# Kernel optimization log

Hardware: AMD Instinct MI355X
Metric: run time of the kernel (lower is better)

## Reference

```python
import jax, jax.numpy as jnp
import numpy as np

B, N, DIM = 16, 1024, 512
H, DH = 8, 64  # heads, dim_head; inner_dim = H*DH = 512
MASK_VAL = -1e-9  # value ASSIGNED (not added) to diagonal, per original code


def setup_inputs() -> dict:
    key = jax.random.key(0)
    ks = jax.random.split(key, 8)
    w = 0.02  # small init so softmax is not saturated
    x = jax.random.normal(ks[0], (B, N, DIM), dtype=jnp.float32)
    Wq = jax.random.normal(ks[1], (DIM, H * DH), dtype=jnp.float32) * w
    Wkv = jax.random.normal(ks[2], (DIM, 2 * H * DH), dtype=jnp.float32) * w
    scale = jnp.full((H,), DH ** -0.5, dtype=jnp.float32)  # nn.Parameter(scale*ones(heads))
    mix_pre = jax.random.normal(ks[3], (H, H), dtype=jnp.float32) * w
    mix_post = jax.random.normal(ks[4], (H, H), dtype=jnp.float32) * w
    Wout = jax.random.normal(ks[5], (H * DH, DIM), dtype=jnp.float32) * w
    bout = jnp.zeros((DIM,), dtype=jnp.float32)
    return {"x": x, "Wq": Wq, "Wkv": Wkv, "scale": scale,
            "mix_pre": mix_pre, "mix_post": mix_post, "Wout": Wout, "bout": bout}


def reference(x, Wq, Wkv, scale, mix_pre, mix_post, Wout, bout):
    b, n, _ = x.shape
    # projections -> [b, h, n, d]
    q = (x @ Wq).reshape(b, n, H, DH).transpose(0, 2, 1, 3)
    kv = (x @ Wkv).reshape(b, n, 2, H, DH)
    k = kv[:, :, 0].transpose(0, 2, 1, 3)
    v = kv[:, :, 1].transpose(0, 2, 1, 3)
    # LMSA: per-head learned scale
    dots = jnp.einsum('bhid,bhjd->bhij', q, k) * scale[None, :, None, None]
    # if_patch_attn: set diagonal entries to -1e-9 (assignment, as in torch)
    eye = jnp.eye(n, dtype=bool)
    dots = jnp.where(eye, jnp.float32(MASK_VAL), dots)
    # talking heads: pre-softmax head mix
    dots = jnp.einsum('bhij,hg->bgij', dots, mix_pre)
    attn = jax.nn.softmax(dots, axis=-1)
    # post-softmax head mix
    attn = jnp.einsum('bhij,hg->bgij', attn, mix_post)
    out = jnp.einsum('bhij,bhjd->bhid', attn, v)  # [b,h,n,d]
    out = out.transpose(0, 2, 1, 3).reshape(b, n, H * DH)
    return out @ Wout + bout
```

## Files before the change

kernel.cpp:

```cpp
#include <hip/hip_runtime.h>
#include <math.h>


typedef short bf16x8 __attribute__((ext_vector_type(8)));
typedef float f32x4 __attribute__((ext_vector_type(4)));

__device__ __forceinline__ f32x4 mfma16(bf16x8 a, bf16x8 b, f32x4 c) {
  return __builtin_amdgcn_mfma_f32_16x16x32_bf16(a, b, c, 0, 0, 0);
}

__device__ __forceinline__ unsigned short f2bf(float f) {
  unsigned u = __float_as_uint(f);
  u = (u + 0x7fffu + ((u >> 16) & 1u)) >> 16;
  return (unsigned short)u;
}

__device__ __forceinline__ void splitbf(float f, unsigned short& hi,
                                        unsigned short& lo) {
  hi = f2bf(f);
  float fh = __uint_as_float((unsigned)hi << 16);
  lo = f2bf(f - fh);
}

__device__ __forceinline__ f32x4 zero4() {
  f32x4 z = {0.f, 0.f, 0.f, 0.f};
  return z;
}

namespace {

constexpr int kB = 16, kN = 1024, kH = 8;

__global__ __launch_bounds__(256) void zero_f32(float* __restrict__ p) {
  int id = blockIdx.x * 256 + threadIdx.x;
  ((float4*)p)[id] = make_float4(0.f, 0.f, 0.f, 0.f);
}

__global__ __launch_bounds__(256) void prep(
    const float* __restrict__ Wq, const float* __restrict__ Wkv,
    const float* __restrict__ Wout, unsigned short* __restrict__ WTh,
    unsigned short* __restrict__ WTl, unsigned short* __restrict__ WoTh,
    unsigned short* __restrict__ WoTl) {
  int id = blockIdx.x * 256 + threadIdx.x;
  unsigned short h, l;
  if (id < 1536 * 512) {
    int n = id >> 9, k = id & 511;
    float v = (n < 512) ? Wq[(size_t)k * 512 + n]
                        : Wkv[(size_t)k * 1024 + (n - 512)];
    splitbf(v, h, l);
    WTh[id] = h; WTl[id] = l;
  } else {
    int id2 = id - 1536 * 512;
    int n = id2 >> 9, k = id2 & 511;
    splitbf(Wout[(size_t)k * 512 + n], h, l);
    WoTh[id2] = h; WoTl[id2] = l;
  }
}

__global__ __launch_bounds__(256) void gemm_qkv(
    const float* __restrict__ X, const unsigned short* __restrict__ WTh,
    const unsigned short* __restrict__ WTl, const float* __restrict__ scale,
    unsigned short* __restrict__ Qh, unsigned short* __restrict__ Ql,
    unsigned short* __restrict__ Kh, unsigned short* __restrict__ Kl,
    unsigned short* __restrict__ Vh, unsigned short* __restrict__ Vl) {
  __shared__ unsigned short Ah[128 * 72], Al[128 * 72];
  __shared__ unsigned short Bh[128 * 72], Bl[128 * 72];
  const int tid = threadIdx.x;
  const int n0 = blockIdx.x * 128, m0 = blockIdx.y * 128;
  const int w = tid >> 6, lane = tid & 63, quad = lane >> 4, ln = lane & 15;
  const int mw = (w >> 1) * 64, nw = (w & 1) * 64;
  const int srow = tid >> 3, schk = (tid & 7) * 8;
  f32x4 acc[4][4];
#pragma unroll
  for (int i = 0; i < 4; ++i)
#pragma unroll
    for (int j = 0; j < 4; ++j) acc[i][j] = zero4();
  for (int k0 = 0; k0 < 512; k0 += 64) {
    float xa[4][8];
    uint4 bh4[4], bl4[4];
#pragma unroll
    for (int c2 = 0; c2 < 4; ++c2) {
      const float* xs = X + (size_t)(m0 + c2 * 32 + srow) * 512 + k0 + schk;
      *(float4*)&xa[c2][0] = *(const float4*)xs;
      *(float4*)&xa[c2][4] = *(const float4*)(xs + 4);
      size_t boff = (size_t)(n0 + c2 * 32 + srow) * 512 + k0 + schk;
      bh4[c2] = *(const uint4*)(WTh + boff);
      bl4[c2] = *(const uint4*)(WTl + boff);
    }
    __syncthreads();
#pragma unroll
    for (int c2 = 0; c2 < 4; ++c2) {
      unsigned short hh[8], ll[8];
#pragma unroll
      for (int e = 0; e < 8; ++e) splitbf(xa[c2][e], hh[e], ll[e]);
      uint4 ph, pl;
      ph.x = hh[0] | ((unsigned)hh[1] << 16); pl.x = ll[0] | ((unsigned)ll[1] << 16);
      ph.y = hh[2] | ((unsigned)hh[3] << 16); pl.y = ll[2] | ((unsigned)ll[3] << 16);
      ph.z = hh[4] | ((unsigned)hh[5] << 16); pl.z = ll[4] | ((unsigned)ll[5] << 16);
      ph.w = hh[6] | ((unsigned)hh[7] << 16); pl.w = ll[6] | ((unsigned)ll[7] << 16);
      *(uint4*)&Ah[(c2 * 32 + srow) * 72 + schk] = ph;
      *(uint4*)&Al[(c2 * 32 + srow) * 72 + schk] = pl;
      *(uint4*)&Bh[(c2 * 32 + srow) * 72 + schk] = bh4[c2];
      *(uint4*)&Bl[(c2 * 32 + srow) * 72 + schk] = bl4[c2];
    }
    __syncthreads();
#pragma unroll
    for (int ks = 0; ks < 2; ++ks) {
      bf16x8 afh[4], afl[4], bfh[4], bfl[4];
#pragma unroll
      for (int t = 0; t < 4; ++t) {
        int ao = (mw + t * 16 + ln) * 72 + ks * 32 + quad * 8;
        int bo = (nw + t * 16 + ln) * 72 + ks * 32 + quad * 8;
        afh[t] = *(const bf16x8*)&Ah[ao];
        afl[t] = *(const bf16x8*)&Al[ao];
        bfh[t] = *(const bf16x8*)&Bh[bo];
        bfl[t] = *(const bf16x8*)&Bl[bo];
      }
#pragma unroll
      for (int mt = 0; mt < 4; ++mt)
#pragma unroll
        for (int nt = 0; nt < 4; ++nt) {
          acc[mt][nt] = mfma16(afh[mt], bfh[nt], acc[mt][nt]);
          acc[mt][nt] = mfma16(afh[mt], bfl[nt], acc[mt][nt]);
          acc[mt][nt] = mfma16(afl[mt], bfh[nt], acc[mt][nt]);
        }
    }
  }
  const int region = n0 >> 9;
#pragma unroll
  for (int nt = 0; nt < 4; ++nt) {
    const int col = n0 + nw + nt * 16 + ln;
    const int local = col - region * 512;
    const int hh = local >> 6, d = local & 63;
    const float sc = (region == 0) ? scale[hh] : 1.f;
#pragma unroll
    for (int mt = 0; mt < 4; ++mt) {
#pragma unroll
      for (int r = 0; r < 4; ++r) {
        const int row = m0 + mw + mt * 16 + quad * 4 + r;
        const int b = row >> 10, i = row & 1023;
        unsigned short vh, vl;
        splitbf(acc[mt][nt][r] * sc, vh, vl);
        if (region == 0) {
          size_t o = (((size_t)(b * 8 + hh) * 1024 + i) << 6) + d;
          Qh[o] = vh; Ql[o] = vl;
        } else if (region == 1) {
          size_t o = (((size_t)(b * 8 + hh) * 1024 + i) << 6) + d;
          Kh[o] = vh; Kl[o] = vl;
        } else {
          size_t o = (((size_t)(b * 8 + hh) * 64 + d) << 10) + i;
          Vh[o] = vh; Vl[o] = vl;
        }
      }
    }
  }
}

__global__ __launch_bounds__(256) void attn_stats(
    const unsigned short* __restrict__ Qh_g, const unsigned short* __restrict__ Ql_g,
    const unsigned short* __restrict__ Kh, const unsigned short* __restrict__ Kl,
    const float* __restrict__ mix_pre, float* __restrict__ Lst) {
  __shared__ unsigned short Qsh[256 * 72];
  __shared__ float mixp_s[64], dfix_s[8];
  const int tid = threadIdx.x;
  const int b = blockIdx.y;
  const int i0 = (blockIdx.x >> 1) * 32;
  const int jb = (blockIdx.x & 1) * 512;
  const int w = tid >> 6, lane = tid & 63, quad = lane >> 4, ln = lane & 15;
  const int ih = (w >> 1) * 16, jh = (w & 1) * 16;
  if (tid < 64) mixp_s[tid] = mix_pre[tid];
  if (tid < 8) {
    float s = 0.f;
#pragma unroll
    for (int h = 0; h < 8; ++h) s += mix_pre[h * 8 + tid];
    dfix_s[tid] = -1e-9f * s;
  }
#pragma unroll
  for (int c = 0; c < 8; ++c) {
    int v = tid + 256 * c;
    int row = v >> 3, chk = (v & 7) * 8;
    int h = row >> 5, ii = row & 31;
    *(uint4*)&Qsh[row * 72 + chk] =
        *(const uint4*)(Qh_g + (((size_t)(b * 8 + h) * 1024 + i0 + ii) << 6) + chk);
  }
  bf16x8 qlo[8][2];
#pragma unroll
  for (int h = 0; h < 8; ++h)
#pragma unroll
    for (int ks = 0; ks < 2; ++ks)
      qlo[h][ks] = *(const bf16x8*)(
          Ql_g + (((size_t)(b * 8 + h) * 1024 + i0 + ih + ln) << 6) + ks * 32 + quad * 8);
  __syncthreads();
  float l[8][4];
#pragma unroll
  for (int a = 0; a < 8; ++a)
#pragma unroll
    for (int r = 0; r < 4; ++r) l[a][r] = 0.f;
  const int ig0 = i0 + ih + quad * 4;
  for (int j0 = jb; j0 < jb + 512; j0 += 32) {
    bf16x8 kh_r[2][2], kl_r[2][2];
#pragma unroll
    for (int ks = 0; ks < 2; ++ks) {
      size_t kro = (((size_t)(b * 8 + 0) * 1024 + j0 + jh + ln) << 6) + ks * 32 + quad * 8;
      kh_r[0][ks] = *(const bf16x8*)(Kh + kro);
      kl_r[0][ks] = *(const bf16x8*)(Kl + kro);
    }
    f32x4 S[8];
    int cur = 0;
#pragma unroll
    for (int h = 0; h < 8; ++h) {
      const int nxt = cur ^ 1;
      if (h < 7) {
#pragma unroll
        for (int ks = 0; ks < 2; ++ks) {
          size_t kro = (((size_t)(b * 8 + h + 1) * 1024 + j0 + jh + ln) << 6) + ks * 32 + quad * 8;
          kh_r[nxt][ks] = *(const bf16x8*)(Kh + kro);
          kl_r[nxt][ks] = *(const bf16x8*)(Kl + kro);
        }
      }
      f32x4 acc = zero4();
#pragma unroll
      for (int ks = 0; ks < 2; ++ks) {
        bf16x8 ah = *(const bf16x8*)&Qsh[(h * 32 + ih + ln) * 72 + ks * 32 + quad * 8];
        acc = mfma16(ah, kh_r[cur][ks], acc);
        acc = mfma16(ah, kl_r[cur][ks], acc);
        acc = mfma16(qlo[h][ks], kh_r[cur][ks], acc);
      }
      S[h] = acc;
      cur = nxt;
    }
    const int dr = (j0 + jh + ln) - ig0;
#pragma unroll
    for (int a = 0; a < 8; ++a) {
      f32x4 sm = S[0] * mixp_s[a];
#pragma unroll
      for (int h = 1; h < 8; ++h) sm += S[h] * mixp_s[h * 8 + a];
      const float df = dfix_s[a];
#pragma unroll
      for (int r = 0; r < 4; ++r) {
        float v = (r == dr) ? df : sm[r];
        l[a][r] += __expf(v);
      }
    }
  }
#pragma unroll
  for (int off = 1; off < 16; off <<= 1)
#pragma unroll
    for (int a = 0; a < 8; ++a)
#pragma unroll
      for (int r = 0; r < 4; ++r) l[a][r] += __shfl_xor(l[a][r], off);
  if (ln == 0) {
#pragma unroll
    for (int a = 0; a < 8; ++a)
#pragma unroll
      for (int r = 0; r < 4; ++r)
        atomicAdd(&Lst[(size_t)(b * 8 + a) * 1024 + ig0 + r], l[a][r]);
  }
}

__global__ __launch_bounds__(256) void attn_out(
    const unsigned short* __restrict__ Qh_g, const unsigned short* __restrict__ Ql_g,
    const unsigned short* __restrict__ Kh, const unsigned short* __restrict__ Kl,
    const unsigned short* __restrict__ Vh, const unsigned short* __restrict__ Vl,
    const float* __restrict__ mix_pre, const float* __restrict__ mix_post,
    const float* __restrict__ Lst, float* __restrict__ OAp) {
  __shared__ unsigned short Qsh[256 * 72];
  __shared__ unsigned short Wsh[256 * 40], Wsl[256 * 40];
  __shared__ float mixp_s[64], mixq_s[64], dfix_s[8];
  __shared__ float Ils[8][32];
  const int tid = threadIdx.x;
  const int b = blockIdx.y;
  const int i0 = (blockIdx.x >> 1) * 32;
  const int jb = (blockIdx.x & 1) * 512;
  float* OA = OAp + (size_t)(blockIdx.x & 1) * ((size_t)kB * kN * 512);
  const int w = tid >> 6, lane = tid & 63, quad = lane >> 4, ln = lane & 15;
  const int ih = (w >> 1) * 16, jh = (w & 1) * 16;
  if (tid < 64) { mixp_s[tid] = mix_pre[tid]; mixq_s[tid] = mix_post[tid]; }
  if (tid < 8) {
    float s = 0.f;
#pragma unroll
    for (int h = 0; h < 8; ++h) s += mix_pre[h * 8 + tid];
    dfix_s[tid] = -1e-9f * s;
  }
  {
    const int a = tid >> 5, row = tid & 31;
    Ils[a][row] = 1.f / Lst[(size_t)(b * 8 + a) * 1024 + i0 + row];
  }
#pragma unroll
  for (int c = 0; c < 8; ++c) {
    int v = tid + 256 * c;
    int row = v >> 3, chk = (v & 7) * 8;
    int h = row >> 5, ii = row & 31;
    *(uint4*)&Qsh[row * 72 + chk] =
        *(const uint4*)(Qh_g + (((size_t)(b * 8 + h) * 1024 + i0 + ii) << 6) + chk);
  }
  bf16x8 qlo[8][2];
#pragma unroll
  for (int h = 0; h < 8; ++h)
#pragma unroll
    for (int ks = 0; ks < 2; ++ks)
      qlo[h][ks] = *(const bf16x8*)(
          Ql_g + (((size_t)(b * 8 + h) * 1024 + i0 + ih + ln) << 6) + ks * 32 + quad * 8);
  __syncthreads();
  f32x4 O[2][2][4];
#pragma unroll
  for (int cc = 0; cc < 2; ++cc)
#pragma unroll
    for (int mt = 0; mt < 2; ++mt)
#pragma unroll
      for (int nt = 0; nt < 4; ++nt) O[cc][mt][nt] = zero4();
  const int ig0l = ih + quad * 4;
  for (int j0 = jb; j0 < jb + 512; j0 += 32) {
    bf16x8 kh_r[2][2], kl_r[2][2];
#pragma unroll
    for (int ks = 0; ks < 2; ++ks) {
      size_t kro = (((size_t)(b * 8 + 0) * 1024 + j0 + jh + ln) << 6) + ks * 32 + quad * 8;
      kh_r[0][ks] = *(const bf16x8*)(Kh + kro);
      kl_r[0][ks] = *(const bf16x8*)(Kl + kro);
    }
    f32x4 S[8];
    int cur = 0;
#pragma unroll
    for (int h = 0; h < 8; ++h) {
      const int nxt = cur ^ 1;
      if (h < 7) {
#pragma unroll
        for (int ks = 0; ks < 2; ++ks) {
          size_t kro = (((size_t)(b * 8 + h + 1) * 1024 + j0 + jh + ln) << 6) + ks * 32 + quad * 8;
          kh_r[nxt][ks] = *(const bf16x8*)(Kh + kro);
          kl_r[nxt][ks] = *(const bf16x8*)(Kl + kro);
        }
      }
      f32x4 acc = zero4();
#pragma unroll
      for (int ks = 0; ks < 2; ++ks) {
        bf16x8 ah = *(const bf16x8*)&Qsh[(h * 32 + ih + ln) * 72 + ks * 32 + quad * 8];
        acc = mfma16(ah, kh_r[cur][ks], acc);
        acc = mfma16(ah, kl_r[cur][ks], acc);
        acc = mfma16(qlo[h][ks], kh_r[cur][ks], acc);
      }
      S[h] = acc;
      cur = nxt;
    }
    const int dr = (j0 + jh + ln) - (i0 + ig0l);
    f32x4 P[8];
#pragma unroll
    for (int a = 0; a < 8; ++a) {
      f32x4 sm = S[0] * mixp_s[a];
#pragma unroll
      for (int h = 1; h < 8; ++h) sm += S[h] * mixp_s[h * 8 + a];
      const float df = dfix_s[a];
      f32x4 p;
#pragma unroll
      for (int r = 0; r < 4; ++r) {
        float v = (r == dr) ? df : sm[r];
        p[r] = __expf(v) * Ils[a][ig0l + r];
      }
      P[a] = p;
    }
#pragma unroll
    for (int c = 0; c < 8; ++c) {
      f32x4 wv = P[0] * mixq_s[c];
#pragma unroll
      for (int a = 1; a < 8; ++a) wv += P[a] * mixq_s[a * 8 + c];
#pragma unroll
      for (int r = 0; r < 4; ++r) {
        unsigned short vh, vl;
        splitbf(wv[r], vh, vl);
        int o = (c * 32 + ig0l + r) * 40 + jh + ln;
        Wsh[o] = vh; Wsl[o] = vl;
      }
    }
    __syncthreads();
#pragma unroll
    for (int cc = 0; cc < 2; ++cc) {
      const int c = w * 2 + cc;
      bf16x8 a0h = *(const bf16x8*)&Wsh[(c * 32 + ln) * 40 + quad * 8];
      bf16x8 a0l = *(const bf16x8*)&Wsl[(c * 32 + ln) * 40 + quad * 8];
      bf16x8 a1h = *(const bf16x8*)&Wsh[(c * 32 + 16 + ln) * 40 + quad * 8];
      bf16x8 a1l = *(const bf16x8*)&Wsl[(c * 32 + 16 + ln) * 40 + quad * 8];
#pragma unroll
      for (int nt = 0; nt < 4; ++nt) {
        size_t vo = (((size_t)(b * 8 + c) * 64 + nt * 16 + ln) << 10) + j0 + quad * 8;
        bf16x8 bvh = *(const bf16x8*)(Vh + vo);
        bf16x8 bvl = *(const bf16x8*)(Vl + vo);
        O[cc][0][nt] = mfma16(a0h, bvh, O[cc][0][nt]);
        O[cc][0][nt] = mfma16(a0h, bvl, O[cc][0][nt]);
        O[cc][0][nt] = mfma16(a0l, bvh, O[cc][0][nt]);
        O[cc][1][nt] = mfma16(a1h, bvh, O[cc][1][nt]);
        O[cc][1][nt] = mfma16(a1h, bvl, O[cc][1][nt]);
        O[cc][1][nt] = mfma16(a1l, bvh, O[cc][1][nt]);
      }
    }
    __syncthreads();
  }
#pragma unroll
  for (int cc = 0; cc < 2; ++cc)
#pragma unroll
    for (int mt = 0; mt < 2; ++mt)
#pragma unroll
      for (int nt = 0; nt < 4; ++nt)
#pragma unroll
        for (int r = 0; r < 4; ++r) {
          const int i = i0 + mt * 16 + quad * 4 + r;
          const int col = (w * 2 + cc) * 64 + nt * 16 + ln;
          OA[((size_t)(b * 1024 + i) << 9) + col] = O[cc][mt][nt][r];
        }
}

__global__ __launch_bounds__(256) void gemm_out(
    const float* __restrict__ A0, const float* __restrict__ A1,
    const unsigned short* __restrict__ BTh, const unsigned short* __restrict__ BTl,
    const float* __restrict__ bias, float* __restrict__ Out) {
  __shared__ unsigned short Ah[128 * 72], Al[128 * 72];
  __shared__ unsigned short Bh[128 * 72], Bl[128 * 72];
  const int tid = threadIdx.x;
  const int n0 = blockIdx.x * 128, m0 = blockIdx.y * 128;
  const int w = tid >> 6, lane = tid & 63, quad = lane >> 4, ln = lane & 15;
  const int mw = (w >> 1) * 64, nw = (w & 1) * 64;
  const int srow = tid >> 3, schk = (tid & 7) * 8;
  f32x4 acc[4][4];
#pragma unroll
  for (int i = 0; i < 4; ++i)
#pragma unroll
    for (int j = 0; j < 4; ++j) acc[i][j] = zero4();
  for (int k0 = 0; k0 < 512; k0 += 64) {
    float xa[4][8];
    uint4 bh4[4], bl4[4];
#pragma unroll
    for (int c2 = 0; c2 < 4; ++c2) {
      size_t aoff = (size_t)(m0 + c2 * 32 + srow) * 512 + k0 + schk;
      float4 a00 = *(const float4*)(A0 + aoff);
      float4 a01 = *(const float4*)(A0 + aoff + 4);
      float4 a10 = *(const float4*)(A1 + aoff);
      float4 a11 = *(const float4*)(A1 + aoff + 4);
      xa[c2][0] = a00.x + a10.x; xa[c2][1] = a00.y + a10.y;
      xa[c2][2] = a00.z + a10.z; xa[c2][3] = a00.w + a10.w;
      xa[c2][4] = a01.x + a11.x; xa[c2][5] = a01.y + a11.y;
      xa[c2][6] = a01.z + a11.z; xa[c2][7] = a01.w + a11.w;
      size_t boff = (size_t)(n0 + c2 * 32 + srow) * 512 + k0 + schk;
      bh4[c2] = *(const uint4*)(BTh + boff);
      bl4[c2] = *(const uint4*)(BTl + boff);
    }
    __syncthreads();
#pragma unroll
    for (int c2 = 0; c2 < 4; ++c2) {
      unsigned short hh[8], ll[8];
#pragma unroll
      for (int e = 0; e < 8; ++e) splitbf(xa[c2][e], hh[e], ll[e]);
      uint4 ph, pl;
      ph.x = hh[0] | ((unsigned)hh[1] << 16); pl.x = ll[0] | ((unsigned)ll[1] << 16);
      ph.y = hh[2] | ((unsigned)hh[3] << 16); pl.y = ll[2] | ((unsigned)ll[3] << 16);
      ph.z = hh[4] | ((unsigned)hh[5] << 16); pl.z = ll[4] | ((unsigned)ll[5] << 16);
      ph.w = hh[6] | ((unsigned)hh[7] << 16); pl.w = ll[6] | ((unsigned)ll[7] << 16);
      *(uint4*)&Ah[(c2 * 32 + srow) * 72 + schk] = ph;
      *(uint4*)&Al[(c2 * 32 + srow) * 72 + schk] = pl;
      *(uint4*)&Bh[(c2 * 32 + srow) * 72 + schk] = bh4[c2];
      *(uint4*)&Bl[(c2 * 32 + srow) * 72 + schk] = bl4[c2];
    }
    __syncthreads();
#pragma unroll
    for (int ks = 0; ks < 2; ++ks) {
      bf16x8 afh[4], afl[4], bfh[4], bfl[4];
#pragma unroll
      for (int t = 0; t < 4; ++t) {
        int ao = (mw + t * 16 + ln) * 72 + ks * 32 + quad * 8;
        int bo = (nw + t * 16 + ln) * 72 + ks * 32 + quad * 8;
        afh[t] = *(const bf16x8*)&Ah[ao];
        afl[t] = *(const bf16x8*)&Al[ao];
        bfh[t] = *(const bf16x8*)&Bh[bo];
        bfl[t] = *(const bf16x8*)&Bl[bo];
      }
#pragma unroll
      for (int mt = 0; mt < 4; ++mt)
#pragma unroll
        for (int nt = 0; nt < 4; ++nt) {
          acc[mt][nt] = mfma16(afh[mt], bfh[nt], acc[mt][nt]);
          acc[mt][nt] = mfma16(afh[mt], bfl[nt], acc[mt][nt]);
          acc[mt][nt] = mfma16(afl[mt], bfh[nt], acc[mt][nt]);
        }
    }
  }
#pragma unroll
  for (int nt = 0; nt < 4; ++nt) {
    const int col = n0 + nw + nt * 16 + ln;
    const float bcol = bias[col];
#pragma unroll
    for (int mt = 0; mt < 4; ++mt) {
#pragma unroll
      for (int r = 0; r < 4; ++r) {
        const int row = m0 + mw + mt * 16 + quad * 4 + r;
        Out[(size_t)row * 512 + col] = acc[mt][nt][r] + bcol;
      }
    }
  }
}

}

extern "C" void kernel_launch(void* const* d_in, const int* in_sizes, int n_in,
                              void* d_out, int out_size, void* d_ws, size_t ws_size,
                              hipStream_t stream) {
  const float* x        = (const float*)d_in[0];
  const float* Wq       = (const float*)d_in[1];
  const float* Wkv      = (const float*)d_in[2];
  const float* scale    = (const float*)d_in[3];
  const float* mix_pre  = (const float*)d_in[4];
  const float* mix_post = (const float*)d_in[5];
  const float* Wout     = (const float*)d_in[6];
  const float* bout     = (const float*)d_in[7];
  float* out = (float*)d_out;

  char* p = (char*)d_ws;
  const size_t qsz = (size_t)kB * kH * kN * 64;
  unsigned short* WTh  = (unsigned short*)p; p += (size_t)1536 * 512 * 2;
  unsigned short* WTl  = (unsigned short*)p; p += (size_t)1536 * 512 * 2;
  unsigned short* WoTh = (unsigned short*)p; p += (size_t)512 * 512 * 2;
  unsigned short* WoTl = (unsigned short*)p; p += (size_t)512 * 512 * 2;
  unsigned short* Qh   = (unsigned short*)p; p += qsz * 2;
  unsigned short* Ql   = (unsigned short*)p; p += qsz * 2;
  unsigned short* Kh   = (unsigned short*)p; p += qsz * 2;
  unsigned short* Kl   = (unsigned short*)p; p += qsz * 2;
  unsigned short* Vh   = (unsigned short*)p; p += qsz * 2;
  unsigned short* Vl   = (unsigned short*)p; p += qsz * 2;
  float* OAp = (float*)p; p += (size_t)2 * kB * kN * 512 * 4;
  float* Lst = (float*)p; p += (size_t)kB * kH * kN * 4;

  prep<<<4096, 256, 0, stream>>>(Wq, Wkv, Wout, WTh, WTl, WoTh, WoTl);
  gemm_qkv<<<dim3(12, 128), 256, 0, stream>>>(x, WTh, WTl, scale,
                                              Qh, Ql, Kh, Kl, Vh, Vl);
  zero_f32<<<128, 256, 0, stream>>>(Lst);
  attn_stats<<<dim3(64, 16), 256, 0, stream>>>(Qh, Ql, Kh, Kl, mix_pre, Lst);
  attn_out<<<dim3(64, 16), 256, 0, stream>>>(Qh, Ql, Kh, Kl, Vh, Vl, mix_pre,
                                             mix_post, Lst, OAp);
  gemm_out<<<dim3(4, 128), 256, 0, stream>>>(OAp, OAp + (size_t)kB * kN * 512,
                                             WoTh, WoTl, bout, out);
}
```

Baseline: 1.582 ms.

## Fuse softmax-stats and output attention passes into one kernel per query tile

Merges attn_stats and attn_out into a single kernel. Each 128-thread block now covers 16 query rows and the full key range. Row sums are reduced in shared memory instead of via atomics into a global buffer, which removes the zero-fill kernel, the atomics and the split-j partial output buffers that gemm_out had to add together. The trade-off is fewer threads per block (two waves) with a serial 1024-key loop, so each block does more sequential work and parallelism per block drops. V loads are double-buffered across heads.

```diff
diff --git a/kernel.cpp b/kernel.cpp
--- a/kernel.cpp
+++ b/kernel.cpp
@@ -30,11 +30,6 @@
 namespace {
 
 constexpr int kB = 16, kN = 1024, kH = 8;
-
-__global__ __launch_bounds__(256) void zero_f32(float* __restrict__ p) {
-  int id = blockIdx.x * 256 + threadIdx.x;
-  ((float4*)p)[id] = make_float4(0.f, 0.f, 0.f, 0.f);
-}
 
 __global__ __launch_bounds__(256) void prep(
     const float* __restrict__ Wq, const float* __restrict__ Wkv,
@@ -156,19 +151,22 @@
   }
 }
 
-__global__ __launch_bounds__(256) void attn_stats(
+__global__ __launch_bounds__(128) void attn_fused(
     const unsigned short* __restrict__ Qh_g, const unsigned short* __restrict__ Ql_g,
     const unsigned short* __restrict__ Kh, const unsigned short* __restrict__ Kl,
-    const float* __restrict__ mix_pre, float* __restrict__ Lst) {
-  __shared__ unsigned short Qsh[256 * 72];
-  __shared__ float mixp_s[64], dfix_s[8];
+    const unsigned short* __restrict__ Vh, const unsigned short* __restrict__ Vl,
+    const float* __restrict__ mix_pre, const float* __restrict__ mix_post,
+    float* __restrict__ OA) {
+  __shared__ unsigned short Qsh[128 * 72];
+  __shared__ unsigned short Wsh[128 * 40], Wsl[128 * 40];
+  __shared__ float mixp_s[64], mixq_s[64], dfix_s[8];
+  __shared__ float Ils[8][16];
+  float* lred = (float*)Wsh;
   const int tid = threadIdx.x;
-  const int b = blockIdx.y;
-  const int i0 = (blockIdx.x >> 1) * 32;
-  const int jb = (blockIdx.x & 1) * 512;
+  const int b = blockIdx.y, i0 = blockIdx.x * 16;
   const int w = tid >> 6, lane = tid & 63, quad = lane >> 4, ln = lane & 15;
-  const int ih = (w >> 1) * 16, jh = (w & 1) * 16;
-  if (tid < 64) mixp_s[tid] = mix_pre[tid];
+  const int jh = w * 16;
+  if (tid < 64) { mixp_s[tid] = mix_pre[tid]; mixq_s[tid] = mix_post[tid]; }
   if (tid < 8) {
     float s = 0.f;
 #pragma unroll
@@ -177,9 +175,9 @@
   }
 #pragma unroll
   for (int c = 0; c < 8; ++c) {
-    int v = tid + 256 * c;
+    int v = tid + 128 * c;
     int row = v >> 3, chk = (v & 7) * 8;
-    int h = row >> 5, ii = row & 31;
+    int h = row >> 4, ii = row & 15;
     *(uint4*)&Qsh[row * 72 + chk] =
         *(const uint4*)(Qh_g + (((size_t)(b * 8 + h) * 1024 + i0 + ii) << 6) + chk);
   }
@@ -189,15 +187,16 @@
 #pragma unroll
     for (int ks = 0; ks < 2; ++ks)
       qlo[h][ks] = *(const bf16x8*)(
-          Ql_g + (((size_t)(b * 8 + h) * 1024 + i0 + ih + ln) << 6) + ks * 32 + quad * 8);
+          Ql_g + (((size_t)(b * 8 + h) * 1024 + i0 + ln) << 6) + ks * 32 + quad * 8);
   __syncthreads();
+  const int ig0 = i0 + quad * 4;
+
   float l[8][4];
 #pragma unroll
   for (int a = 0; a < 8; ++a)
 #pragma unroll
     for (int r = 0; r < 4; ++r) l[a][r] = 0.f;
-  const int ig0 = i0 + ih + quad * 4;
-  for (int j0 = jb; j0 < jb + 512; j0 += 32) {
+  for (int j0 = 0; j0 < 1024; j0 += 32) {
     bf16x8 kh_r[2][2], kl_r[2][2];
 #pragma unroll
     for (int ks = 0; ks < 2; ++ks) {
@@ -221,7 +220,7 @@
       f32x4 acc = zero4();
 #pragma unroll
       for (int ks = 0; ks < 2; ++ks) {
-        bf16x8 ah = *(const bf16x8*)&Qsh[(h * 32 + ih + ln) * 72 + ks * 32 + quad * 8];
+        bf16x8 ah = *(const bf16x8*)&Qsh[(h * 16 + ln) * 72 + ks * 32 + quad * 8];
         acc = mfma16(ah, kh_r[cur][ks], acc);
         acc = mfma16(ah, kl_r[cur][ks], acc);
         acc = mfma16(qlo[h][ks], kh_r[cur][ks], acc);
@@ -253,64 +252,21 @@
 #pragma unroll
     for (int a = 0; a < 8; ++a)
 #pragma unroll
-      for (int r = 0; r < 4; ++r)
-        atomicAdd(&Lst[(size_t)(b * 8 + a) * 1024 + ig0 + r], l[a][r]);
-  }
-}
-
-__global__ __launch_bounds__(256) void attn_out(
-    const unsigned short* __restrict__ Qh_g, const unsigned short* __restrict__ Ql_g,
-    const unsigned short* __restrict__ Kh, const unsigned short* __restrict__ Kl,
-    const unsigned short* __restrict__ Vh, const unsigned short* __restrict__ Vl,
-    const float* __restrict__ mix_pre, const float* __restrict__ mix_post,
-    const float* __restrict__ Lst, float* __restrict__ OAp) {
-  __shared__ unsigned short Qsh[256 * 72];
-  __shared__ unsigned short Wsh[256 * 40], Wsl[256 * 40];
-  __shared__ float mixp_s[64], mixq_s[64], dfix_s[8];
-  __shared__ float Ils[8][32];
-  const int tid = threadIdx.x;
-  const int b = blockIdx.y;
-  const int i0 = (blockIdx.x >> 1) * 32;
-  const int jb = (blockIdx.x & 1) * 512;
-  float* OA = OAp + (size_t)(blockIdx.x & 1) * ((size_t)kB * kN * 512);
-  const int w = tid >> 6, lane = tid & 63, quad = lane >> 4, ln = lane & 15;
-  const int ih = (w >> 1) * 16, jh = (w & 1) * 16;
-  if (tid < 64) { mixp_s[tid] = mix_pre[tid]; mixq_s[tid] = mix_post[tid]; }
-  if (tid < 8) {
-    float s = 0.f;
-#pragma unroll
-    for (int h = 0; h < 8; ++h) s += mix_pre[h * 8 + tid];
-    dfix_s[tid] = -1e-9f * s;
-  }
+      for (int r = 0; r < 4; ++r) lred[(w * 8 + a) * 16 + quad * 4 + r] = l[a][r];
+  }
+  __syncthreads();
   {
-    const int a = tid >> 5, row = tid & 31;
-    Ils[a][row] = 1.f / Lst[(size_t)(b * 8 + a) * 1024 + i0 + row];
-  }
-#pragma unroll
-  for (int c = 0; c < 8; ++c) {
-    int v = tid + 256 * c;
-    int row = v >> 3, chk = (v & 7) * 8;
-    int h = row >> 5, ii = row & 31;
-    *(uint4*)&Qsh[row * 72 + chk] =
-        *(const uint4*)(Qh_g + (((size_t)(b * 8 + h) * 1024 + i0 + ii) << 6) + chk);
-  }
-  bf16x8 qlo[8][2];
-#pragma unroll
-  for (int h = 0; h < 8; ++h)
-#pragma unroll
-    for (int ks = 0; ks < 2; ++ks)
-      qlo[h][ks] = *(const bf16x8*)(
-          Ql_g + (((size_t)(b * 8 + h) * 1024 + i0 + ih + ln) << 6) + ks * 32 + quad * 8);
+    int a = tid >> 4, i = tid & 15;
+    Ils[a][i] = 1.f / (lred[a * 16 + i] + lred[(8 + a) * 16 + i]);
+  }
   __syncthreads();
-  f32x4 O[2][2][4];
-#pragma unroll
-  for (int cc = 0; cc < 2; ++cc)
-#pragma unroll
-    for (int mt = 0; mt < 2; ++mt)
-#pragma unroll
-      for (int nt = 0; nt < 4; ++nt) O[cc][mt][nt] = zero4();
-  const int ig0l = ih + quad * 4;
-  for (int j0 = jb; j0 < jb + 512; j0 += 32) {
+
+  f32x4 O[4][4];
+#pragma unroll
+  for (int cc = 0; cc < 4; ++cc)
+#pragma unroll
+    for (int nt = 0; nt < 4; ++nt) O[cc][nt] = zero4();
+  for (int j0 = 0; j0 < 1024; j0 += 32) {
     bf16x8 kh_r[2][2], kl_r[2][2];
 #pragma unroll
     for (int ks = 0; ks < 2; ++ks) {
@@ -334,7 +290,7 @@
       f32x4 acc = zero4();
 #pragma unroll
       for (int ks = 0; ks < 2; ++ks) {
-        bf16x8 ah = *(const bf16x8*)&Qsh[(h * 32 + ih + ln) * 72 + ks * 32 + quad * 8];
+        bf16x8 ah = *(const bf16x8*)&Qsh[(h * 16 + ln) * 72 + ks * 32 + quad * 8];
         acc = mfma16(ah, kh_r[cur][ks], acc);
         acc = mfma16(ah, kl_r[cur][ks], acc);
         acc = mfma16(qlo[h][ks], kh_r[cur][ks], acc);
@@ -342,7 +298,7 @@
       S[h] = acc;
       cur = nxt;
     }
-    const int dr = (j0 + jh + ln) - (i0 + ig0l);
+    const int dr = (j0 + jh + ln) - ig0;
     f32x4 P[8];
 #pragma unroll
     for (int a = 0; a < 8; ++a) {
@@ -350,11 +306,12 @@
 #pragma unroll
       for (int h = 1; h < 8; ++h) sm += S[h] * mixp_s[h * 8 + a];
       const float df = dfix_s[a];
+      f32x4 il4 = *(const f32x4*)&Ils[a][quad * 4];
       f32x4 p;
 #pragma unroll
       for (int r = 0; r < 4; ++r) {
         float v = (r == dr) ? df : sm[r];
-        p[r] = __expf(v) * Ils[a][ig0l + r];
+        p[r] = __expf(v) * il4[r];
       }
       P[a] = p;
     }
@@ -367,51 +324,62 @@
       for (int r = 0; r < 4; ++r) {
         unsigned short vh, vl;
         splitbf(wv[r], vh, vl);
-        int o = (c * 32 + ig0l + r) * 40 + jh + ln;
+        int o = (c * 16 + quad * 4 + r) * 40 + jh + ln;
         Wsh[o] = vh; Wsl[o] = vl;
       }
     }
-    __syncthreads();
-#pragma unroll
-    for (int cc = 0; cc < 2; ++cc) {
-      const int c = w * 2 + cc;
-      bf16x8 a0h = *(const bf16x8*)&Wsh[(c * 32 + ln) * 40 + quad * 8];
-      bf16x8 a0l = *(const bf16x8*)&Wsl[(c * 32 + ln) * 40 + quad * 8];
-      bf16x8 a1h = *(const bf16x8*)&Wsh[(c * 32 + 16 + ln) * 40 + quad * 8];
-      bf16x8 a1l = *(const bf16x8*)&Wsl[(c * 32 + 16 + ln) * 40 + quad * 8];
+    bf16x8 vbh[2][4], vbl[2][4];
+    {
+      const int c = w * 4;
 #pragma unroll
       for (int nt = 0; nt < 4; ++nt) {
         size_t vo = (((size_t)(b * 8 + c) * 64 + nt * 16 + ln) << 10) + j0 + quad * 8;
-        bf16x8 bvh = *(const bf16x8*)(Vh + vo);
-        bf16x8 bvl = *(const bf16x8*)(Vl + vo);
-        O[cc][0][nt] = mfma16(a0h, bvh, O[cc][0][nt]);
-        O[cc][0][nt] = mfma16(a0h, bvl, O[cc][0][nt]);
-        O[cc][0][nt] = mfma16(a0l, bvh, O[cc][0][nt]);
-        O[cc][1][nt] = mfma16(a1h, bvh, O[cc][1][nt]);
-        O[cc][1][nt] = mfma16(a1h, bvl, O[cc][1][nt]);
-        O[cc][1][nt] = mfma16(a1l, bvh, O[cc][1][nt]);
-      }
-    }
-    __syncthreads();
-  }
-#pragma unroll
-  for (int cc = 0; cc < 2; ++cc)
-#pragma unroll
-    for (int mt = 0; mt < 2; ++mt)
-#pragma unroll
-      for (int nt = 0; nt < 4; ++nt)
-#pragma unroll
-        for (int r = 0; r < 4; ++r) {
-          const int i = i0 + mt * 16 + quad * 4 + r;
-          const int col = (w * 2 + cc) * 64 + nt * 16 + ln;
-          OA[((size_t)(b * 1024 + i) << 9) + col] = O[cc][mt][nt][r];
-        }
+        vbh[0][nt] = *(const bf16x8*)(Vh + vo);
+        vbl[0][nt] = *(const bf16x8*)(Vl + vo);
+      }
+    }
+    __syncthreads();
+    int vcur = 0;
+#pragma unroll
+    for (int cc = 0; cc < 4; ++cc) {
+      const int c = w * 4 + cc;
+      const int vnxt = vcur ^ 1;
+      if (cc < 3) {
+#pragma unroll
+        for (int nt = 0; nt < 4; ++nt) {
+          size_t vo = (((size_t)(b * 8 + c + 1) * 64 + nt * 16 + ln) << 10) + j0 + quad * 8;
+          vbh[vnxt][nt] = *(const bf16x8*)(Vh + vo);
+          vbl[vnxt][nt] = *(const bf16x8*)(Vl + vo);
+        }
+      }
+      bf16x8 a_h = *(const bf16x8*)&Wsh[(c * 16 + ln) * 40 + quad * 8];
+      bf16x8 a_l = *(const bf16x8*)&Wsl[(c * 16 + ln) * 40 + quad * 8];
+#pragma unroll
+      for (int nt = 0; nt < 4; ++nt) {
+        O[cc][nt] = mfma16(a_h, vbh[vcur][nt], O[cc][nt]);
+        O[cc][nt] = mfma16(a_h, vbl[vcur][nt], O[cc][nt]);
+        O[cc][nt] = mfma16(a_l, vbh[vcur][nt], O[cc][nt]);
+      }
+      vcur = vnxt;
+    }
+    __syncthreads();
+  }
+#pragma unroll
+  for (int cc = 0; cc < 4; ++cc)
+#pragma unroll
+    for (int nt = 0; nt < 4; ++nt)
+#pragma unroll
+      for (int r = 0; r < 4; ++r) {
+        const int i = i0 + quad * 4 + r;
+        const int col = (w * 4 + cc) * 64 + nt * 16 + ln;
+        OA[((size_t)(b * 1024 + i) << 9) + col] = O[cc][nt][r];
+      }
 }
 
 __global__ __launch_bounds__(256) void gemm_out(
-    const float* __restrict__ A0, const float* __restrict__ A1,
-    const unsigned short* __restrict__ BTh, const unsigned short* __restrict__ BTl,
-    const float* __restrict__ bias, float* __restrict__ Out) {
+    const float* __restrict__ A, const unsigned short* __restrict__ BTh,
+    const unsigned short* __restrict__ BTl, const float* __restrict__ bias,
+    float* __restrict__ Out) {
   __shared__ unsigned short Ah[128 * 72], Al[128 * 72];
   __shared__ unsigned short Bh[128 * 72], Bl[128 * 72];
   const int tid = threadIdx.x;
@@ -429,15 +397,9 @@
     uint4 bh4[4], bl4[4];
 #pragma unroll
     for (int c2 = 0; c2 < 4; ++c2) {
-      size_t aoff = (size_t)(m0 + c2 * 32 + srow) * 512 + k0 + schk;
-      float4 a00 = *(const float4*)(A0 + aoff);
-      float4 a01 = *(const float4*)(A0 + aoff + 4);
-      float4 a10 = *(const float4*)(A1 + aoff);
-      float4 a11 = *(const float4*)(A1 + aoff + 4);
-      xa[c2][0] = a00.x + a10.x; xa[c2][1] = a00.y + a10.y;
-      xa[c2][2] = a00.z + a10.z; xa[c2][3] = a00.w + a10.w;
-      xa[c2][4] = a01.x + a11.x; xa[c2][5] = a01.y + a11.y;
-      xa[c2][6] = a01.z + a11.z; xa[c2][7] = a01.w + a11.w;
+      const float* xs = A + (size_t)(m0 + c2 * 32 + srow) * 512 + k0 + schk;
+      *(float4*)&xa[c2][0] = *(const float4*)xs;
+      *(float4*)&xa[c2][4] = *(const float4*)(xs + 4);
       size_t boff = (size_t)(n0 + c2 * 32 + srow) * 512 + k0 + schk;
       bh4[c2] = *(const uint4*)(BTh + boff);
       bl4[c2] = *(const uint4*)(BTl + boff);
@@ -523,16 +485,12 @@
   unsigned short* Kl   = (unsigned short*)p; p += qsz * 2;
   unsigned short* Vh   = (unsigned short*)p; p += qsz * 2;
   unsigned short* Vl   = (unsigned short*)p; p += qsz * 2;
-  float* OAp = (float*)p; p += (size_t)2 * kB * kN * 512 * 4;
-  float* Lst = (float*)p; p += (size_t)kB * kH * kN * 4;
+  float* OA = (float*)p; p += (size_t)kB * kN * 512 * 4;
 
   prep<<<4096, 256, 0, stream>>>(Wq, Wkv, Wout, WTh, WTl, WoTh, WoTl);
   gemm_qkv<<<dim3(12, 128), 256, 0, stream>>>(x, WTh, WTl, scale,
                                               Qh, Ql, Kh, Kl, Vh, Vl);
-  zero_f32<<<128, 256, 0, stream>>>(Lst);
-  attn_stats<<<dim3(64, 16), 256, 0, stream>>>(Qh, Ql, Kh, Kl, mix_pre, Lst);
-  attn_out<<<dim3(64, 16), 256, 0, stream>>>(Qh, Ql, Kh, Kl, Vh, Vl, mix_pre,
-                                             mix_post, Lst, OAp);
-  gemm_out<<<dim3(4, 128), 256, 0, stream>>>(OAp, OAp + (size_t)kB * kN * 512,
-                                             WoTh, WoTl, bout, out);
-}
+  attn_fused<<<dim3(64, 16), 128, 0, stream>>>(Qh, Ql, Kh, Kl, Vh, Vl,
+                                               mix_pre, mix_post, OA);
+  gemm_out<<<dim3(4, 128), 256, 0, stream>>>(OA, WoTh, WoTl, bout, out);
+}
```

After: 1.435 ms. 9.3% less time.
